# Performance work log

Measured on AMD Instinct MI355X. Metric: run time of the kernel, lower is better.

## Reference

```python
import jax, jax.numpy as jnp
import numpy as np

B, T, DM, H, D = 2, 4096, 1024, 16, 64
HD = H * D
PHASE_SCALE = 10.0


def _multiscale_phasors(num_heads, head_dim):
    # Deterministic multiscale frequencies: RoPE-like geometric spacing over
    # the feature dim, with a per-head octave scale (reconstruction of the
    # registered buffer `freqs` from generate_multiscale_phasors).
    d = np.arange(head_dim, dtype=np.float32) / head_dim
    base = 10000.0 ** (-d)                      # (D,)
    head_scale = 2.0 ** (-np.arange(num_heads, dtype=np.float32))  # (H,)
    return jnp.asarray(2.0 * np.pi * head_scale[:, None] * base[None, :],
                       dtype=jnp.float32)       # (H, D)


def setup_inputs() -> dict:
    key = jax.random.key(0)
    k0, k1, k2, k3 = jax.random.split(key, 4)
    x = jax.random.normal(k0, (B, T, DM), jnp.float32)
    Wk = jax.random.normal(k1, (DM, HD), jnp.float32) / np.float32(np.sqrt(DM))
    Wv = jax.random.normal(k2, (DM, HD), jnp.float32) / np.float32(np.sqrt(DM))
    Wo = jax.random.normal(k3, (HD, DM), jnp.float32) / np.float32(np.sqrt(HD))
    gate = jnp.full((H, 2), 0.5, jnp.float32)
    freqs = _multiscale_phasors(H, D)
    return {"x": x, "Wk": Wk, "Wv": Wv, "Wo": Wo, "gate": gate, "freqs": freqs}


def _holo_fused_step(v, binder, probe):
    # (cumsum(v * binder, dim=1) * probe).real / sqrt(1..T)
    mem = jnp.cumsum(v * binder, axis=1)                     # (B,T,H,D) complex64
    t = v.shape[1]
    scale = jnp.sqrt(jnp.arange(1, t + 1, dtype=jnp.float32))[None, :, None, None]
    return jnp.real(mem * probe) / scale                     # (B,T,H,D) float32


def reference(x, Wk, Wv, Wo, gate, freqs):
    Bb, Tt, _ = x.shape
    k_real = (x @ Wk).reshape(Bb, Tt, H, D)                  # (B,T,H,D)
    v = (x @ Wv).reshape(Bb, Tt, H, D).astype(jnp.complex64)
    k = jnp.exp(1j * (k_real * PHASE_SCALE))                 # unit phasors, q = k
    # Positional path: rotors = exp(i * t * freqs)
    t = jnp.arange(Tt, dtype=jnp.float32)
    rotors = jnp.exp(1j * (t[:, None, None] * freqs))[None]  # (1,T,H,D)
    out_pos = _holo_fused_step(v, rotors, jnp.conj(rotors))
    # Associative path: bind with conj of shifted keys, retrieve with q=k
    k_shifted = jnp.roll(k, 1, axis=1).at[:, 0].set(0.0)
    out_assoc = _holo_fused_step(v, jnp.conj(k_shifted), k)
    g_pos = gate[:, 0][None, None, :, None]
    g_assoc = gate[:, 1][None, None, :, None]
    out = out_pos * g_pos + out_assoc * g_assoc              # (B,T,H,D)
    return out.reshape(Bb, Tt, HD) @ Wo                      # dropout p=0 -> identity
```

## Files before the change

kernel.cpp:

```cpp
#include <hip/hip_runtime.h>


#define B_ 2
#define T_ 4096
#define H_ 16
#define D_ 64
#define M_ (B_*T_)
#define PHASE_SCALE 10.0f

typedef _Float16 f16;
typedef unsigned int u32;
typedef __attribute__((ext_vector_type(8))) _Float16 f16x8;
typedef __attribute__((ext_vector_type(4))) _Float16 f16x4;
typedef __attribute__((ext_vector_type(4))) float f32x4;


__global__ void k_cvt_f32_f16(const float* __restrict__ src, f16* __restrict__ dst, int n) {
  int idx = (blockIdx.x * blockDim.x + threadIdx.x) * 4;
  if (idx < n) {
    float4 v = *reinterpret_cast<const float4*>(src + idx);
    f16x4 o;
    o[0] = (f16)v.x; o[1] = (f16)v.y; o[2] = (f16)v.z; o[3] = (f16)v.w;
    *reinterpret_cast<f16x4*>(dst + idx) = o;
  }
}

__global__ void k_transpose_cvt(const float* __restrict__ src, f16* __restrict__ dst) {
  __shared__ float tile[32][33];
  int bx = blockIdx.x, by = blockIdx.y;
  int tx = threadIdx.x, ty = threadIdx.y;
  #pragma unroll
  for (int r = 0; r < 32; r += 8)
    tile[ty + r][tx] = src[(size_t)(by * 32 + ty + r) * 1024 + bx * 32 + tx];
  __syncthreads();
  #pragma unroll
  for (int r = 0; r < 32; r += 8)
    dst[(size_t)(bx * 32 + ty + r) * 1024 + by * 32 + tx] = (f16)tile[tx][ty + r];
}


__device__ __forceinline__ void gl2lds16(const f16* g, char* l) {
  __builtin_amdgcn_global_load_lds((const __attribute__((address_space(1))) u32*)g,
                                   (__attribute__((address_space(3))) u32*)l, 16, 0, 0);
}

#define S_BAR() __builtin_amdgcn_s_barrier()
#define WAIT_LGKM0() do { asm volatile("s_waitcnt lgkmcnt(0)" ::: "memory"); \
                          __builtin_amdgcn_sched_barrier(0); } while (0)
#define WAIT_VM(n) asm volatile("s_waitcnt vmcnt(" #n ")" ::: "memory")

#define STAGE(gp, ldsoff, kkt) do { \
  gl2lds16((gp) + (size_t)(kkt) * 64,               smem + (ldsoff) + tid * 16); \
  gl2lds16((gp) + (size_t)(kkt) * 64 + 64 * 1024,   smem + (ldsoff) + 8192 + tid * 16); \
} while (0)

#define PHASE(AH, BH, READ_A, VMW, STG) do { \
  if (READ_A) { \
    _Pragma("unroll") for (int mi = 0; mi < 4; ++mi) \
    _Pragma("unroll") for (int kk = 0; kk < 2; ++kk) \
      aF[mi][kk] = *(const f16x8*)(smem + curbuf + (AH) * 16384 + offA[mi][kk]); \
  } \
  _Pragma("unroll") for (int nj = 0; nj < 2; ++nj) \
  _Pragma("unroll") for (int kk = 0; kk < 2; ++kk) \
    bF[nj][kk] = *(const f16x8*)(smem + curbuf + 32768 + (BH) * 16384 + offB[nj][kk]); \
  STG; \
  S_BAR(); \
  WAIT_LGKM0(); \
  __builtin_amdgcn_s_setprio(1); \
  _Pragma("unroll") for (int mi = 0; mi < 4; ++mi) \
  _Pragma("unroll") for (int nj = 0; nj < 2; ++nj) \
  _Pragma("unroll") for (int kk = 0; kk < 2; ++kk) \
    acc[(AH) * 2 + (BH)][mi][nj] = __builtin_amdgcn_mfma_f32_16x16x32_f16( \
        aF[mi][kk], bF[nj][kk], acc[(AH) * 2 + (BH)][mi][nj], 0, 0, 0); \
  __builtin_amdgcn_s_setprio(0); \
  VMW; \
  S_BAR(); \
} while (0)

__launch_bounds__(512, 1)
__global__ void k_gemm8(const f16* __restrict__ A, const f16* __restrict__ Bt,
                        float* __restrict__ C32, f16* __restrict__ C16) {
  extern __shared__ char smem[];
  const int tid  = threadIdx.x;
  const int lane = tid & 63;
  const int wid  = tid >> 6;
  const int wr   = wid >> 2, wc = wid & 3;
  const int lr   = lane & 15, hi = lane >> 4;
  const int m0   = blockIdx.x * 256;
  const int n0   = blockIdx.y * 256;

  const int rsub = tid >> 3;
  const int csw  = ((tid & 7) ^ (rsub & 7)) * 8;
  const f16* gA0 = A  + (size_t)(m0 + rsub) * 1024 + csw;
  const f16* gA1 = gA0 + (size_t)128 * 1024;
  const f16* gB0 = Bt + (size_t)(n0 + rsub) * 1024 + csw;
  const f16* gB1 = gB0 + (size_t)128 * 1024;

  int offA[4][2], offB[2][2];
  #pragma unroll
  for (int mi = 0; mi < 4; ++mi)
    #pragma unroll
    for (int kk = 0; kk < 2; ++kk) {
      int row = wr * 64 + mi * 16 + lr;
      offA[mi][kk] = row * 128 + (((kk * 4 + hi) ^ (row & 7)) << 4);
    }
  #pragma unroll
  for (int nj = 0; nj < 2; ++nj)
    #pragma unroll
    for (int kk = 0; kk < 2; ++kk) {
      int row = wc * 32 + nj * 16 + lr;
      offB[nj][kk] = row * 128 + (((kk * 4 + hi) ^ (row & 7)) << 4);
    }

  f32x4 acc[4][4][2] = {};
  f16x8 aF[4][2], bF[2][2];

  STAGE(gA0, 0,     0);
  STAGE(gB0, 32768, 0);
  STAGE(gA1, 16384, 0);
  STAGE(gA0, 65536, 1);
  STAGE(gB1, 49152, 0);
  STAGE(gB0, 98304, 1);
  WAIT_VM(8);
  S_BAR();

  for (int kt = 0; kt < 14; ++kt) {
    const int curbuf = (kt & 1) * 65536;
    const int nxtbuf = curbuf ^ 65536;
    PHASE(0, 0, 1, WAIT_VM(4),  STAGE(gA1, nxtbuf + 16384, kt + 1));
    PHASE(0, 1, 0, WAIT_VM(10), STAGE(gA0, curbuf + 0,     kt + 2));
    PHASE(1, 0, 1, (void)0,     STAGE(gB1, nxtbuf + 49152, kt + 1));
    PHASE(1, 1, 0, WAIT_VM(8),  STAGE(gB0, curbuf + 32768, kt + 2));
  }
  {
    const int curbuf = 0, nxtbuf = 65536;
    PHASE(0, 0, 1, WAIT_VM(4), STAGE(gA1, nxtbuf + 16384, 15));
    PHASE(0, 1, 0, WAIT_VM(8), (void)0);
    PHASE(1, 0, 1, (void)0,    STAGE(gB1, nxtbuf + 49152, 15));
    PHASE(1, 1, 0, WAIT_VM(4), (void)0);
  }
  {
    const int curbuf = 65536;
    PHASE(0, 0, 1, WAIT_VM(0), (void)0);
    PHASE(0, 1, 0, (void)0,    (void)0);
    PHASE(1, 0, 1, (void)0,    (void)0);
    PHASE(1, 1, 0, (void)0,    (void)0);
  }

  const int rb = hi * 4;
  #pragma unroll
  for (int ah = 0; ah < 2; ++ah)
    #pragma unroll
    for (int bh = 0; bh < 2; ++bh)
      #pragma unroll
      for (int mi = 0; mi < 4; ++mi)
        #pragma unroll
        for (int nj = 0; nj < 2; ++nj) {
          f32x4 a4 = acc[ah * 2 + bh][mi][nj];
          const int row = m0 + ah * 128 + wr * 64 + mi * 16 + rb;
          const int col = n0 + bh * 128 + wc * 32 + nj * 16 + lr;
          if (col < 1024) {
            #pragma unroll
            for (int r = 0; r < 4; ++r)
              C32[(size_t)(row + r) * 1024 + col] = a4[r];
          } else {
            #pragma unroll
            for (int r = 0; r < 4; ++r)
              C16[(size_t)(row + r) * 1024 + (col - 1024)] = (f16)a4[r];
          }
        }
}


__global__ void k_scan_part(const float* __restrict__ kf, const f16* __restrict__ vh,
                            const float* __restrict__ freqs, float4* __restrict__ tot) {
  const int bid = blockIdx.x;
  const int cg = bid & 31;
  const int h  = (bid >> 5) & 15;
  const int b  = bid >> 9;
  const int w  = threadIdx.x >> 6;
  const int d  = threadIdx.x & 63;
  const int c  = cg * 4 + w;
  const int t0 = c * 32;
  const int col = h * 64 + d;
  const float f = freqs[col];

  float bc = 0.f, bs = 0.f;
  if (t0 > 0) {
    float krp = kf[(size_t)(b * T_ + t0 - 1) * 1024 + col];
    __sincosf(PHASE_SCALE * krp, &bs, &bc);
  }
  double rev = (double)t0 * (double)f * 0.15915494309189535;
  rev -= floor(rev);
  float ph = (float)rev * 6.28318530717958647692f;
  float ri, rc; __sincosf(ph, &ri, &rc);
  float sf, cf; __sincosf(f, &sf, &cf);

  float pr = 0.f, pi = 0.f, ar = 0.f, ai = 0.f;
  #pragma unroll 8
  for (int tt = 0; tt < 32; ++tt) {
    size_t row = (size_t)(b * T_ + t0 + tt) * 1024 + col;
    float v  = (float)vh[row];
    float kr = kf[row];
    pr = fmaf(v, rc, pr); pi = fmaf(v, ri, pi);
    ar = fmaf(v, bc, ar); ai = fmaf(-v, bs, ai);
    __sincosf(PHASE_SCALE * kr, &bs, &bc);
    float nrc = rc * cf - ri * sf;
    ri = rc * sf + ri * cf; rc = nrc;
  }
  tot[((size_t)(c * 2 + b) * 16 + h) * 64 + d] = make_float4(pr, pi, ar, ai);
}

__global__ void k_scan_carry(const float4* __restrict__ tot, float4* __restrict__ carry) {
  const int h = blockIdx.x & 15;
  const int b = blockIdx.x >> 4;
  const int d = threadIdx.x;
  float pr = 0.f, pi = 0.f, ar = 0.f, ai = 0.f;
  for (int c = 0; c < 128; ++c) {
    size_t idx = ((size_t)(c * 2 + b) * 16 + h) * 64 + d;
    float4 tv = tot[idx];
    carry[idx] = make_float4(pr, pi, ar, ai);
    pr += tv.x; pi += tv.y; ar += tv.z; ai += tv.w;
  }
}

__global__ void k_scan_out(const float* __restrict__ kf, const f16* __restrict__ vh,
                           const float* __restrict__ freqs, const float4* __restrict__ carry,
                           const float* __restrict__ gate, f16* __restrict__ y) {
  const int bid = blockIdx.x;
  const int cg = bid & 31;
  const int h  = (bid >> 5) & 15;
  const int b  = bid >> 9;
  const int w  = threadIdx.x >> 6;
  const int d  = threadIdx.x & 63;
  const int c  = cg * 4 + w;
  const int t0 = c * 32;
  const int col = h * 64 + d;
  const float f = freqs[col];
  const float gp = gate[2 * h], ga = gate[2 * h + 1];

  float4 cr = carry[((size_t)(c * 2 + b) * 16 + h) * 64 + d];
  float pr = cr.x, pi = cr.y, ar = cr.z, ai = cr.w;
  float bc = 0.f, bs = 0.f;
  if (t0 > 0) {
    float krp = kf[(size_t)(b * T_ + t0 - 1) * 1024 + col];
    __sincosf(PHASE_SCALE * krp, &bs, &bc);
  }
  double rev = (double)t0 * (double)f * 0.15915494309189535;
  rev -= floor(rev);
  float ph = (float)rev * 6.28318530717958647692f;
  float ri, rc; __sincosf(ph, &ri, &rc);
  float sf, cf; __sincosf(f, &sf, &cf);

  #pragma unroll 8
  for (int tt = 0; tt < 32; ++tt) {
    int t = t0 + tt;
    size_t row = (size_t)(b * T_ + t) * 1024 + col;
    float v  = (float)vh[row];
    float kr = kf[row];
    pr = fmaf(v, rc, pr); pi = fmaf(v, ri, pi);
    ar = fmaf(v, bc, ar); ai = fmaf(-v, bs, ai);
    float kc, ks; __sincosf(PHASE_SCALE * kr, &ks, &kc);
    float inv = rsqrtf((float)(t + 1));
    float op = fmaf(pr, rc, pi * ri) * inv;
    float oa = fmaf(ar, kc, -(ai * ks)) * inv;
    y[row] = (f16)(gp * op + ga * oa);
    bs = ks; bc = kc;
    float nrc = rc * cf - ri * sf;
    ri = rc * sf + ri * cf; rc = nrc;
  }
}


extern "C" void kernel_launch(void* const* d_in, const int* in_sizes, int n_in,
                              void* d_out, int out_size, void* d_ws, size_t ws_size,
                              hipStream_t stream) {
  const float* x     = (const float*)d_in[0];
  const float* Wk    = (const float*)d_in[1];
  const float* Wv    = (const float*)d_in[2];
  const float* Wo    = (const float*)d_in[3];
  const float* gate  = (const float*)d_in[4];
  const float* freqs = (const float*)d_in[5];
  float* out = (float*)d_out;

  char* ws = (char*)d_ws;
  size_t off = 0;
  auto alloc = [&](size_t bytes) { void* p = ws + off; off += (bytes + 255) & ~255ull; return p; };

  f16*    xh    = (f16*)   alloc((size_t)M_ * 1024 * sizeof(f16));
  f16*    Wkvt  = (f16*)   alloc((size_t)2048 * 1024 * sizeof(f16));
  f16*    Wot   = (f16*)   alloc((size_t)1024 * 1024 * sizeof(f16));
  float*  kf    = (float*) alloc((size_t)M_ * 1024 * sizeof(float));
  f16*    vh    = (f16*)   alloc((size_t)M_ * 1024 * sizeof(f16));
  float4* tot   = (float4*)alloc((size_t)128 * B_ * H_ * D_ * sizeof(float4));
  float4* carry = (float4*)alloc((size_t)128 * B_ * H_ * D_ * sizeof(float4));
  f16*    yh    = xh;

  hipFuncSetAttribute(reinterpret_cast<const void*>(&k_gemm8),
                      hipFuncAttributeMaxDynamicSharedMemorySize, 131072);

  hipLaunchKernelGGL(k_cvt_f32_f16, dim3((M_ * 1024 / 4 + 255) / 256), dim3(256), 0, stream,
                     x, xh, M_ * 1024);
  hipLaunchKernelGGL(k_transpose_cvt, dim3(32, 32), dim3(32, 8), 0, stream, Wk, Wkvt);
  hipLaunchKernelGGL(k_transpose_cvt, dim3(32, 32), dim3(32, 8), 0, stream, Wv, Wkvt + (size_t)1024 * 1024);
  hipLaunchKernelGGL(k_transpose_cvt, dim3(32, 32), dim3(32, 8), 0, stream, Wo, Wot);
  hipLaunchKernelGGL(k_gemm8, dim3(32, 8), dim3(512), 131072, stream, xh, Wkvt, kf, vh);
  hipLaunchKernelGGL(k_scan_part,  dim3(1024), dim3(256), 0, stream, kf, vh, freqs, tot);
  hipLaunchKernelGGL(k_scan_carry, dim3(32),   dim3(64),  0, stream, tot, carry);
  hipLaunchKernelGGL(k_scan_out,   dim3(1024), dim3(256), 0, stream, kf, vh, freqs, carry, gate, yh);
  hipLaunchKernelGGL(k_gemm8, dim3(32, 4), dim3(512), 131072, stream, yh, Wot, out, nullptr);
}
```

Measured before the change: 203.1 us.

## Fuse prep kernels, drop scan carry kernel, templatize GEMM tile height

Merges the f32-to-f16 conversion of x and the three weight transposes into one launch. It also removes the separate carry kernel: each scan_out block now sums the preceding chunk totals itself, and the scan chunk length grows from 32 to 64 steps. The GEMM becomes a template on tile height, so the output projection uses 128-row tiles (256 blocks instead of 128) for better CU fill, and B fragments are cached across phases. The cost is redundant prefix-sum work per block, longer serial scan chains with fewer blocks, and more complex pipeline wait counts.

```diff
diff --git a/kernel.cpp b/kernel.cpp
--- a/kernel.cpp
+++ b/kernel.cpp
@@ -15,20 +15,27 @@
 typedef __attribute__((ext_vector_type(4))) float f32x4;
 
 
-__global__ void k_cvt_f32_f16(const float* __restrict__ src, f16* __restrict__ dst, int n) {
-  int idx = (blockIdx.x * blockDim.x + threadIdx.x) * 4;
-  if (idx < n) {
-    float4 v = *reinterpret_cast<const float4*>(src + idx);
-    f16x4 o;
-    o[0] = (f16)v.x; o[1] = (f16)v.y; o[2] = (f16)v.z; o[3] = (f16)v.w;
-    *reinterpret_cast<f16x4*>(dst + idx) = o;
-  }
-}
-
-__global__ void k_transpose_cvt(const float* __restrict__ src, f16* __restrict__ dst) {
+__global__ void k_prep(const float* __restrict__ x, const float* __restrict__ Wk,
+                       const float* __restrict__ Wv, const float* __restrict__ Wo,
+                       f16* __restrict__ xh, f16* __restrict__ Wkvt, f16* __restrict__ Wot) {
   __shared__ float tile[32][33];
-  int bx = blockIdx.x, by = blockIdx.y;
-  int tx = threadIdx.x, ty = threadIdx.y;
+  const int z = blockIdx.z;
+  const int tx = threadIdx.x, ty = threadIdx.y;
+  if (z == 3) {
+    const int blk = blockIdx.y * 32 + blockIdx.x;
+    const size_t base = (size_t)blk * 256 + ty * 32 + tx;
+    #pragma unroll
+    for (int i = 0; i < 8; ++i) {
+      size_t idx = (base + (size_t)i * 262144) * 4;
+      float4 v = *reinterpret_cast<const float4*>(x + idx);
+      f16x4 o; o[0] = (f16)v.x; o[1] = (f16)v.y; o[2] = (f16)v.z; o[3] = (f16)v.w;
+      *reinterpret_cast<f16x4*>(xh + idx) = o;
+    }
+    return;
+  }
+  const float* src = (z == 0) ? Wk : (z == 1) ? Wv : Wo;
+  f16* dst = (z == 0) ? Wkvt : (z == 1) ? (Wkvt + (size_t)1024 * 1024) : Wot;
+  const int bx = blockIdx.x, by = blockIdx.y;
   #pragma unroll
   for (int r = 0; r < 32; r += 8)
     tile[ty + r][tx] = src[(size_t)(by * 32 + ty + r) * 1024 + bx * 32 + tx];
@@ -49,59 +56,70 @@
                           __builtin_amdgcn_sched_barrier(0); } while (0)
 #define WAIT_VM(n) asm volatile("s_waitcnt vmcnt(" #n ")" ::: "memory")
 
-#define STAGE(gp, ldsoff, kkt) do { \
-  gl2lds16((gp) + (size_t)(kkt) * 64,               smem + (ldsoff) + tid * 16); \
-  gl2lds16((gp) + (size_t)(kkt) * 64 + 64 * 1024,   smem + (ldsoff) + 8192 + tid * 16); \
+#define STAGE_A(gp, ldsoff, kkt) do { \
+  gl2lds16((gp) + (size_t)(kkt) * 64, smem + (ldsoff) + tid * 16); \
+  if constexpr (MI == 4) \
+    gl2lds16((gp) + (size_t)(kkt) * 64 + 64 * 1024, smem + (ldsoff) + 8192 + tid * 16); \
 } while (0)
-
-#define PHASE(AH, BH, READ_A, VMW, STG) do { \
+#define STAGE_B(gp, ldsoff, kkt) do { \
+  gl2lds16((gp) + (size_t)(kkt) * 64, smem + (ldsoff) + tid * 16); \
+  gl2lds16((gp) + (size_t)(kkt) * 64 + 64 * 1024, smem + (ldsoff) + 8192 + tid * 16); \
+} while (0)
+
+#define PHASE(AH, BH, READ_A, READ_B, VMW, STG) do { \
   if (READ_A) { \
-    _Pragma("unroll") for (int mi = 0; mi < 4; ++mi) \
+    _Pragma("unroll") for (int mi = 0; mi < MI; ++mi) \
     _Pragma("unroll") for (int kk = 0; kk < 2; ++kk) \
-      aF[mi][kk] = *(const f16x8*)(smem + curbuf + (AH) * 16384 + offA[mi][kk]); \
+      aF[mi][kk] = *(const f16x8*)(smem + curbuf + (AH) * AHB + offA[mi][kk]); \
   } \
-  _Pragma("unroll") for (int nj = 0; nj < 2; ++nj) \
-  _Pragma("unroll") for (int kk = 0; kk < 2; ++kk) \
-    bF[nj][kk] = *(const f16x8*)(smem + curbuf + 32768 + (BH) * 16384 + offB[nj][kk]); \
+  if (READ_B) { \
+    _Pragma("unroll") for (int nj = 0; nj < 2; ++nj) \
+    _Pragma("unroll") for (int kk = 0; kk < 2; ++kk) \
+      bF[BH][nj][kk] = *(const f16x8*)(smem + curbuf + 2 * AHB + (BH) * 16384 + offB[nj][kk]); \
+  } \
   STG; \
   S_BAR(); \
   WAIT_LGKM0(); \
   __builtin_amdgcn_s_setprio(1); \
-  _Pragma("unroll") for (int mi = 0; mi < 4; ++mi) \
+  _Pragma("unroll") for (int mi = 0; mi < MI; ++mi) \
   _Pragma("unroll") for (int nj = 0; nj < 2; ++nj) \
   _Pragma("unroll") for (int kk = 0; kk < 2; ++kk) \
     acc[(AH) * 2 + (BH)][mi][nj] = __builtin_amdgcn_mfma_f32_16x16x32_f16( \
-        aF[mi][kk], bF[nj][kk], acc[(AH) * 2 + (BH)][mi][nj], 0, 0, 0); \
+        aF[mi][kk], bF[BH][nj][kk], acc[(AH) * 2 + (BH)][mi][nj], 0, 0, 0); \
   __builtin_amdgcn_s_setprio(0); \
   VMW; \
   S_BAR(); \
 } while (0)
 
+template<int MI>
 __launch_bounds__(512, 1)
 __global__ void k_gemm8(const f16* __restrict__ A, const f16* __restrict__ Bt,
                         float* __restrict__ C32, f16* __restrict__ C16) {
   extern __shared__ char smem[];
+  constexpr int AH_R = MI * 32;
+  constexpr int AHB  = AH_R * 128;
+  constexpr int BUFSZ = 2 * AHB + 32768;
   const int tid  = threadIdx.x;
   const int lane = tid & 63;
   const int wid  = tid >> 6;
   const int wr   = wid >> 2, wc = wid & 3;
   const int lr   = lane & 15, hi = lane >> 4;
-  const int m0   = blockIdx.x * 256;
+  const int m0   = blockIdx.x * (MI * 64);
   const int n0   = blockIdx.y * 256;
 
   const int rsub = tid >> 3;
   const int csw  = ((tid & 7) ^ (rsub & 7)) * 8;
   const f16* gA0 = A  + (size_t)(m0 + rsub) * 1024 + csw;
-  const f16* gA1 = gA0 + (size_t)128 * 1024;
+  const f16* gA1 = gA0 + (size_t)AH_R * 1024;
   const f16* gB0 = Bt + (size_t)(n0 + rsub) * 1024 + csw;
   const f16* gB1 = gB0 + (size_t)128 * 1024;
 
-  int offA[4][2], offB[2][2];
-  #pragma unroll
-  for (int mi = 0; mi < 4; ++mi)
+  int offA[MI][2], offB[2][2];
+  #pragma unroll
+  for (int mi = 0; mi < MI; ++mi)
     #pragma unroll
     for (int kk = 0; kk < 2; ++kk) {
-      int row = wr * 64 + mi * 16 + lr;
+      int row = wr * (MI * 16) + mi * 16 + lr;
       offA[mi][kk] = row * 128 + (((kk * 4 + hi) ^ (row & 7)) << 4);
     }
   #pragma unroll
@@ -112,39 +130,42 @@
       offB[nj][kk] = row * 128 + (((kk * 4 + hi) ^ (row & 7)) << 4);
     }
 
-  f32x4 acc[4][4][2] = {};
-  f16x8 aF[4][2], bF[2][2];
-
-  STAGE(gA0, 0,     0);
-  STAGE(gB0, 32768, 0);
-  STAGE(gA1, 16384, 0);
-  STAGE(gA0, 65536, 1);
-  STAGE(gB1, 49152, 0);
-  STAGE(gB0, 98304, 1);
-  WAIT_VM(8);
+  f32x4 acc[4][MI][2] = {};
+  f16x8 aF[MI][2], bF[2][2][2];
+
+  STAGE_A(gA0, 0,            0);
+  STAGE_B(gB0, 2 * AHB,      0);
+  STAGE_A(gA1, AHB,          0);
+  STAGE_A(gA0, BUFSZ,        1);
+  STAGE_B(gB1, 2 * AHB + 16384, 0);
+  STAGE_B(gB0, BUFSZ + 2 * AHB, 1);
+  if constexpr (MI == 4) WAIT_VM(8); else WAIT_VM(6);
   S_BAR();
 
   for (int kt = 0; kt < 14; ++kt) {
-    const int curbuf = (kt & 1) * 65536;
-    const int nxtbuf = curbuf ^ 65536;
-    PHASE(0, 0, 1, WAIT_VM(4),  STAGE(gA1, nxtbuf + 16384, kt + 1));
-    PHASE(0, 1, 0, WAIT_VM(10), STAGE(gA0, curbuf + 0,     kt + 2));
-    PHASE(1, 0, 1, (void)0,     STAGE(gB1, nxtbuf + 49152, kt + 1));
-    PHASE(1, 1, 0, WAIT_VM(8),  STAGE(gB0, curbuf + 32768, kt + 2));
+    const int curbuf = (kt & 1) * BUFSZ;
+    const int nxtbuf = curbuf ^ BUFSZ;
+    PHASE(0, 0, 1, 1, if constexpr (MI == 4) WAIT_VM(4); else WAIT_VM(3),
+          STAGE_A(gA1, nxtbuf + AHB, kt + 1));
+    PHASE(0, 1, 0, 1, (void)0, STAGE_A(gA0, curbuf, kt + 2));
+    PHASE(1, 0, 1, 0, (void)0, STAGE_B(gB1, nxtbuf + 2 * AHB + 16384, kt + 1));
+    PHASE(1, 1, 0, 0, if constexpr (MI == 4) WAIT_VM(8); else WAIT_VM(6),
+          STAGE_B(gB0, curbuf + 2 * AHB, kt + 2));
   }
   {
-    const int curbuf = 0, nxtbuf = 65536;
-    PHASE(0, 0, 1, WAIT_VM(4), STAGE(gA1, nxtbuf + 16384, 15));
-    PHASE(0, 1, 0, WAIT_VM(8), (void)0);
-    PHASE(1, 0, 1, (void)0,    STAGE(gB1, nxtbuf + 49152, 15));
-    PHASE(1, 1, 0, WAIT_VM(4), (void)0);
+    const int curbuf = 0, nxtbuf = BUFSZ;
+    PHASE(0, 0, 1, 1, if constexpr (MI == 4) WAIT_VM(4); else WAIT_VM(3),
+          STAGE_A(gA1, nxtbuf + AHB, 15));
+    PHASE(0, 1, 0, 1, (void)0, (void)0);
+    PHASE(1, 0, 1, 0, (void)0, STAGE_B(gB1, nxtbuf + 2 * AHB + 16384, 15));
+    PHASE(1, 1, 0, 0, if constexpr (MI == 4) WAIT_VM(4); else WAIT_VM(3), (void)0);
   }
   {
-    const int curbuf = 65536;
-    PHASE(0, 0, 1, WAIT_VM(0), (void)0);
-    PHASE(0, 1, 0, (void)0,    (void)0);
-    PHASE(1, 0, 1, (void)0,    (void)0);
-    PHASE(1, 1, 0, (void)0,    (void)0);
+    const int curbuf = BUFSZ;
+    PHASE(0, 0, 1, 1, WAIT_VM(0), (void)0);
+    PHASE(0, 1, 0, 1, (void)0, (void)0);
+    PHASE(1, 0, 1, 0, (void)0, (void)0);
+    PHASE(1, 1, 0, 0, (void)0, (void)0);
   }
 
   const int rb = hi * 4;
@@ -153,11 +174,11 @@
     #pragma unroll
     for (int bh = 0; bh < 2; ++bh)
       #pragma unroll
-      for (int mi = 0; mi < 4; ++mi)
+      for (int mi = 0; mi < MI; ++mi)
         #pragma unroll
         for (int nj = 0; nj < 2; ++nj) {
           f32x4 a4 = acc[ah * 2 + bh][mi][nj];
-          const int row = m0 + ah * 128 + wr * 64 + mi * 16 + rb;
+          const int row = m0 + ah * AH_R + wr * (MI * 16) + mi * 16 + rb;
           const int col = n0 + bh * 128 + wc * 32 + nj * 16 + lr;
           if (col < 1024) {
             #pragma unroll
@@ -175,13 +196,13 @@
 __global__ void k_scan_part(const float* __restrict__ kf, const f16* __restrict__ vh,
                             const float* __restrict__ freqs, float4* __restrict__ tot) {
   const int bid = blockIdx.x;
-  const int cg = bid & 31;
-  const int h  = (bid >> 5) & 15;
-  const int b  = bid >> 9;
+  const int cg = bid & 15;
+  const int h  = (bid >> 4) & 15;
+  const int b  = bid >> 8;
   const int w  = threadIdx.x >> 6;
   const int d  = threadIdx.x & 63;
   const int c  = cg * 4 + w;
-  const int t0 = c * 32;
+  const int t0 = c * 64;
   const int col = h * 64 + d;
   const float f = freqs[col];
 
@@ -197,8 +218,8 @@
   float sf, cf; __sincosf(f, &sf, &cf);
 
   float pr = 0.f, pi = 0.f, ar = 0.f, ai = 0.f;
-  #pragma unroll 8
-  for (int tt = 0; tt < 32; ++tt) {
+  #pragma unroll 4
+  for (int tt = 0; tt < 64; ++tt) {
     size_t row = (size_t)(b * T_ + t0 + tt) * 1024 + col;
     float v  = (float)vh[row];
     float kr = kf[row];
@@ -211,36 +232,27 @@
   tot[((size_t)(c * 2 + b) * 16 + h) * 64 + d] = make_float4(pr, pi, ar, ai);
 }
 
-__global__ void k_scan_carry(const float4* __restrict__ tot, float4* __restrict__ carry) {
-  const int h = blockIdx.x & 15;
-  const int b = blockIdx.x >> 4;
-  const int d = threadIdx.x;
-  float pr = 0.f, pi = 0.f, ar = 0.f, ai = 0.f;
-  for (int c = 0; c < 128; ++c) {
-    size_t idx = ((size_t)(c * 2 + b) * 16 + h) * 64 + d;
-    float4 tv = tot[idx];
-    carry[idx] = make_float4(pr, pi, ar, ai);
-    pr += tv.x; pi += tv.y; ar += tv.z; ai += tv.w;
-  }
-}
-
 __global__ void k_scan_out(const float* __restrict__ kf, const f16* __restrict__ vh,
-                           const float* __restrict__ freqs, const float4* __restrict__ carry,
+                           const float* __restrict__ freqs, const float4* __restrict__ tot,
                            const float* __restrict__ gate, f16* __restrict__ y) {
   const int bid = blockIdx.x;
-  const int cg = bid & 31;
-  const int h  = (bid >> 5) & 15;
-  const int b  = bid >> 9;
+  const int cg = bid & 15;
+  const int h  = (bid >> 4) & 15;
+  const int b  = bid >> 8;
   const int w  = threadIdx.x >> 6;
   const int d  = threadIdx.x & 63;
   const int c  = cg * 4 + w;
-  const int t0 = c * 32;
+  const int t0 = c * 64;
   const int col = h * 64 + d;
   const float f = freqs[col];
   const float gp = gate[2 * h], ga = gate[2 * h + 1];
 
-  float4 cr = carry[((size_t)(c * 2 + b) * 16 + h) * 64 + d];
-  float pr = cr.x, pi = cr.y, ar = cr.z, ai = cr.w;
+  float pr = 0.f, pi = 0.f, ar = 0.f, ai = 0.f;
+  for (int cc = 0; cc < c; ++cc) {
+    float4 tv = tot[((size_t)(cc * 2 + b) * 16 + h) * 64 + d];
+    pr += tv.x; pi += tv.y; ar += tv.z; ai += tv.w;
+  }
+
   float bc = 0.f, bs = 0.f;
   if (t0 > 0) {
     float krp = kf[(size_t)(b * T_ + t0 - 1) * 1024 + col];
@@ -252,8 +264,8 @@
   float ri, rc; __sincosf(ph, &ri, &rc);
   float sf, cf; __sincosf(f, &sf, &cf);
 
-  #pragma unroll 8
-  for (int tt = 0; tt < 32; ++tt) {
+  #pragma unroll 4
+  for (int tt = 0; tt < 64; ++tt) {
     int t = t0 + tt;
     size_t row = (size_t)(b * T_ + t) * 1024 + col;
     float v  = (float)vh[row];
@@ -287,26 +299,23 @@
   size_t off = 0;
   auto alloc = [&](size_t bytes) { void* p = ws + off; off += (bytes + 255) & ~255ull; return p; };
 
-  f16*    xh    = (f16*)   alloc((size_t)M_ * 1024 * sizeof(f16));
-  f16*    Wkvt  = (f16*)   alloc((size_t)2048 * 1024 * sizeof(f16));
-  f16*    Wot   = (f16*)   alloc((size_t)1024 * 1024 * sizeof(f16));
-  float*  kf    = (float*) alloc((size_t)M_ * 1024 * sizeof(float));
-  f16*    vh    = (f16*)   alloc((size_t)M_ * 1024 * sizeof(f16));
-  float4* tot   = (float4*)alloc((size_t)128 * B_ * H_ * D_ * sizeof(float4));
-  float4* carry = (float4*)alloc((size_t)128 * B_ * H_ * D_ * sizeof(float4));
-  f16*    yh    = xh;
-
-  hipFuncSetAttribute(reinterpret_cast<const void*>(&k_gemm8),
+  f16*    xh   = (f16*)   alloc((size_t)M_ * 1024 * sizeof(f16));
+  f16*    Wkvt = (f16*)   alloc((size_t)2048 * 1024 * sizeof(f16));
+  f16*    Wot  = (f16*)   alloc((size_t)1024 * 1024 * sizeof(f16));
+  float*  kf   = (float*) alloc((size_t)M_ * 1024 * sizeof(float));
+  f16*    vh   = (f16*)   alloc((size_t)M_ * 1024 * sizeof(f16));
+  float4* tot  = (float4*)alloc((size_t)64 * B_ * H_ * D_ * sizeof(float4));
+  f16*    yh   = xh;
+
+  hipFuncSetAttribute(reinterpret_cast<const void*>(&k_gemm8<4>),
                       hipFuncAttributeMaxDynamicSharedMemorySize, 131072);
-
-  hipLaunchKernelGGL(k_cvt_f32_f16, dim3((M_ * 1024 / 4 + 255) / 256), dim3(256), 0, stream,
-                     x, xh, M_ * 1024);
-  hipLaunchKernelGGL(k_transpose_cvt, dim3(32, 32), dim3(32, 8), 0, stream, Wk, Wkvt);
-  hipLaunchKernelGGL(k_transpose_cvt, dim3(32, 32), dim3(32, 8), 0, stream, Wv, Wkvt + (size_t)1024 * 1024);
-  hipLaunchKernelGGL(k_transpose_cvt, dim3(32, 32), dim3(32, 8), 0, stream, Wo, Wot);
-  hipLaunchKernelGGL(k_gemm8, dim3(32, 8), dim3(512), 131072, stream, xh, Wkvt, kf, vh);
-  hipLaunchKernelGGL(k_scan_part,  dim3(1024), dim3(256), 0, stream, kf, vh, freqs, tot);
-  hipLaunchKernelGGL(k_scan_carry, dim3(32),   dim3(64),  0, stream, tot, carry);
-  hipLaunchKernelGGL(k_scan_out,   dim3(1024), dim3(256), 0, stream, kf, vh, freqs, carry, gate, yh);
-  hipLaunchKernelGGL(k_gemm8, dim3(32, 4), dim3(512), 131072, stream, yh, Wot, out, nullptr);
-}
+  hipFuncSetAttribute(reinterpret_cast<const void*>(&k_gemm8<2>),
+                      hipFuncAttributeMaxDynamicSharedMemorySize, 98304);
+
+  hipLaunchKernelGGL(k_prep, dim3(32, 32, 4), dim3(32, 8), 0, stream,
+                     x, Wk, Wv, Wo, xh, Wkvt, Wot);
+  hipLaunchKernelGGL(k_gemm8<4>, dim3(32, 8), dim3(512), 131072, stream, xh, Wkvt, kf, vh);
+  hipLaunchKernelGGL(k_scan_part, dim3(512), dim3(256), 0, stream, kf, vh, freqs, tot);
+  hipLaunchKernelGGL(k_scan_out,  dim3(512), dim3(256), 0, stream, kf, vh, freqs, tot, gate, yh);
+  hipLaunchKernelGGL(k_gemm8<2>, dim3(64, 4), dim3(512), 98304, stream, yh, Wot, out, nullptr);
+}
```

Result: no change. 200.0 us (-1.5%).
